# Performance work log

Hardware: AMD Instinct MI355X
Metric: run time of the kernel (lower is better)

The kernel has to match this reference:

```python
import jax, jax.numpy as jnp
import numpy as np

N = 50000      # nodes
E = 800000     # edges
IN = 64        # in_feats
HID = 4        # hidden_size
OUT = 64       # out_feats
COORS = 3
EPS = 1e-07
NEG_SLOPE = 0.01  # F.leaky_relu default


def setup_inputs() -> dict:
    key = jax.random.key(0)
    ks = jax.random.split(key, 10)
    feat = jax.random.normal(ks[0], (N, IN), dtype=jnp.float32)
    pos = jax.random.normal(ks[1], (N, COORS), dtype=jnp.float32)
    src = jax.random.randint(ks[2], (E,), 0, N, dtype=jnp.int32)
    dst = jax.random.randint(ks[3], (E,), 0, N, dtype=jnp.int32)
    W_self = jax.random.normal(ks[4], (OUT, IN), dtype=jnp.float32) * 0.1
    W_sp = jax.random.normal(ks[5], (HID * IN, COORS), dtype=jnp.float32) * 0.3
    b_sp = jax.random.normal(ks[6], (HID * IN,), dtype=jnp.float32) * 0.05
    W_neigh = jax.random.normal(ks[7], (OUT, HID * IN), dtype=jnp.float32) * 0.05
    b_neigh = jax.random.normal(ks[8], (OUT,), dtype=jnp.float32) * 0.05
    bias = jnp.zeros((OUT,), dtype=jnp.float32)
    return {"feat": feat, "pos": pos, "src": src, "dst": dst,
            "W_self": W_self, "W_sp": W_sp, "b_sp": b_sp,
            "W_neigh": W_neigh, "b_neigh": b_neigh, "bias": bias}


def reference(feat, pos, src, dst, W_self, W_sp, b_sp, W_neigh, b_neigh, bias):
    # per-edge spatial weighting
    rel = pos[dst] - pos[src]                                   # [E, 3]
    scal = jnp.linalg.norm(rel, axis=1, keepdims=True) + EPS    # [E, 1]
    ws = (rel + 1.0) / scal                                     # [E, 3]
    s = jax.nn.leaky_relu(ws @ W_sp.T + b_sp, NEG_SLOPE)        # [E, HID*IN]
    # modulate gathered src features: reshape(E, IN, HID) * h_src[:, :, None]
    msg = (s.reshape(E, IN, HID) * feat[src][:, :, None]).reshape(E, IN * HID)
    # mean aggregation per destination node (zero for isolated nodes)
    neigh_sum = jax.ops.segment_sum(msg, dst, num_segments=N)   # [N, IN*HID]
    cnt = jax.ops.segment_sum(jnp.ones((E,), feat.dtype), dst, num_segments=N)
    neigh_h = neigh_sum / jnp.maximum(cnt, 1.0)[:, None]
    # output projections
    h_neigh = neigh_h @ W_neigh.T + b_neigh                     # [N, OUT]
    rst = feat @ W_self.T + h_neigh + bias                      # [N, OUT]
    return rst
```

## Files before the change

kernel.cpp:

```cpp
#include <hip/hip_runtime.h>
#include <math.h>

#define N_NODES 50000
#define N_EDGES 800000
#define EPS 1e-7f
#define NEG_SLOPE 0.01f

#define BUCKET 64
#define EDGE_BLOCKS (N_EDGES / 256)
#define CNT_STRIDE 16

typedef __attribute__((ext_vector_type(8))) short short8;
typedef __attribute__((ext_vector_type(4))) float f32x4;

__device__ __forceinline__ unsigned bf16_rne(float x) {
    unsigned u = __float_as_uint(x);
    u += 0x7fffu + ((u >> 16) & 1u);
    return u >> 16;
}
__device__ __forceinline__ unsigned pack_bf16(float a, float b) {
    return bf16_rne(a) | (bf16_rne(b) << 16);
}


__global__ __launch_bounds__(256) void prep_kernel(
    const int* __restrict__ src, const int* __restrict__ dst,
    const float* __restrict__ pos,
    int* __restrict__ cnt, uint2* __restrict__ gdata,
    const float* __restrict__ W_neigh, const float* __restrict__ W_self,
    const float* __restrict__ b_neigh, const float* __restrict__ bias,
    unsigned* __restrict__ wnp, unsigned* __restrict__ wsp, float* __restrict__ bb)
{
    const int bid = blockIdx.x;

    if (bid == EDGE_BLOCKS) {
        const int t = threadIdx.x;
        const float2* Wn2 = (const float2*)W_neigh;
        const float2* Ws2 = (const float2*)W_self;
        for (int i = t; i < 64 * 128; i += 256) {
            float2 v = Wn2[i];
            wnp[i] = pack_bf16(v.x, v.y);
        }
        for (int i = t; i < 64 * 32; i += 256) {
            float2 v = Ws2[i];
            wsp[i] = pack_bf16(v.x, v.y);
        }
        if (t < 64) bb[t] = b_neigh[t] + bias[t];
        return;
    }

    const int i = bid * 256 + threadIdx.x;
    const int s = src[i], d = dst[i];
    const float sx = pos[s * 3 + 0], sy = pos[s * 3 + 1], sz = pos[s * 3 + 2];
    const float dx = pos[d * 3 + 0], dy = pos[d * 3 + 1], dz = pos[d * 3 + 2];
    const float rx = dx - sx, ry = dy - sy, rz = dz - sz;
    const float inv =
        __builtin_amdgcn_rcpf(__builtin_amdgcn_sqrtf(rx * rx + ry * ry + rz * rz) + EPS);
    const uint2 rec = make_uint2(pack_bf16((rx + 1.f) * inv, (ry + 1.f) * inv),
                                 bf16_rne((rz + 1.f) * inv) | ((unsigned)s << 16));
    const int p = atomicAdd(&cnt[d * CNT_STRIDE], 1);
    if (p < BUCKET) gdata[(size_t)d * BUCKET + p] = rec;
}


#define ACC_STRIDE 264

__device__ __forceinline__ short8 feat_frag_bf16(const float* p) {
    float4 x0 = *reinterpret_cast<const float4*>(p);
    float4 x1 = *reinterpret_cast<const float4*>(p + 4);
    union { unsigned u[4]; short8 s; } c;
    c.u[0] = pack_bf16(x0.x, x0.y);
    c.u[1] = pack_bf16(x0.z, x0.w);
    c.u[2] = pack_bf16(x1.x, x1.y);
    c.u[3] = pack_bf16(x1.z, x1.w);
    return c.s;
}

__global__ __launch_bounds__(256) void aggregate_project_kernel(
    const float* __restrict__ feat, const float* __restrict__ W_sp,
    const float* __restrict__ b_sp, const int* __restrict__ cnt,
    const uint2* __restrict__ gdata, const short* __restrict__ wnb,
    const short* __restrict__ wsb, const float* __restrict__ bb,
    float* __restrict__ out)
{
    __shared__ unsigned short accS[16 * ACC_STRIDE];

    const int lane = threadIdx.x & 63;
    const int w = threadIdx.x >> 6;
    const int nb = blockIdx.x << 4;

    float wsp0[4], wsp1[4], wsp2[4], bsp[4];
#pragma unroll
    for (int h = 0; h < 4; ++h) {
        int j = lane * 4 + h;
        wsp0[h] = W_sp[j * 3 + 0];
        wsp1[h] = W_sp[j * 3 + 1];
        wsp2[h] = W_sp[j * 3 + 2];
        bsp[h]  = b_sp[j];
    }

    for (int q = 0; q < 4; ++q) {
        const int r = (w << 2) + q;
        const int n = nb + r;
        const int degt = __builtin_amdgcn_readfirstlane(cnt[n * CNT_STRIDE]);
        const int deg = min(degt, BUCKET);
        const uint2* gp = gdata + (size_t)n * BUCKET;

        float a0 = 0.f, a1 = 0.f, a2 = 0.f, a3 = 0.f;

        if (deg > 0) {
            const int dm = deg - 1;
            uint2 u0 = gp[0];
            uint2 u1 = gp[min(1, dm)];
            uint2 u2 = gp[min(2, dm)];
            uint2 u3 = gp[min(3, dm)];
            float f0 = feat[(size_t)(u0.y >> 16) * 64 + lane];
            float f1 = feat[(size_t)(u1.y >> 16) * 64 + lane];

            for (int e = 0; e < deg; e += 2) {
                uint2 u4 = gp[min(e + 4, dm)];
                uint2 u5 = gp[min(e + 5, dm)];
                float f2 = feat[(size_t)(u2.y >> 16) * 64 + lane];
                float f3 = feat[(size_t)(u3.y >> 16) * 64 + lane];

                {
                    const float wx = __uint_as_float(u0.x << 16);
                    const float wy = __uint_as_float(u0.x & 0xffff0000u);
                    const float wz = __uint_as_float(u0.y << 16);
                    float t0 = fmaf(wx, wsp0[0], fmaf(wy, wsp1[0], fmaf(wz, wsp2[0], bsp[0])));
                    float t1 = fmaf(wx, wsp0[1], fmaf(wy, wsp1[1], fmaf(wz, wsp2[1], bsp[1])));
                    float t2 = fmaf(wx, wsp0[2], fmaf(wy, wsp1[2], fmaf(wz, wsp2[2], bsp[2])));
                    float t3 = fmaf(wx, wsp0[3], fmaf(wy, wsp1[3], fmaf(wz, wsp2[3], bsp[3])));
                    a0 = fmaf(fmaxf(t0, t0 * NEG_SLOPE), f0, a0);
                    a1 = fmaf(fmaxf(t1, t1 * NEG_SLOPE), f0, a1);
                    a2 = fmaf(fmaxf(t2, t2 * NEG_SLOPE), f0, a2);
                    a3 = fmaf(fmaxf(t3, t3 * NEG_SLOPE), f0, a3);
                }
                {
                    const float m1 = (e + 1 <= dm) ? 1.f : 0.f;
                    const float fm = f1 * m1;
                    const float wx = __uint_as_float(u1.x << 16);
                    const float wy = __uint_as_float(u1.x & 0xffff0000u);
                    const float wz = __uint_as_float(u1.y << 16);
                    float t0 = fmaf(wx, wsp0[0], fmaf(wy, wsp1[0], fmaf(wz, wsp2[0], bsp[0])));
                    float t1 = fmaf(wx, wsp0[1], fmaf(wy, wsp1[1], fmaf(wz, wsp2[1], bsp[1])));
                    float t2 = fmaf(wx, wsp0[2], fmaf(wy, wsp1[2], fmaf(wz, wsp2[2], bsp[2])));
                    float t3 = fmaf(wx, wsp0[3], fmaf(wy, wsp1[3], fmaf(wz, wsp2[3], bsp[3])));
                    a0 = fmaf(fmaxf(t0, t0 * NEG_SLOPE), fm, a0);
                    a1 = fmaf(fmaxf(t1, t1 * NEG_SLOPE), fm, a1);
                    a2 = fmaf(fmaxf(t2, t2 * NEG_SLOPE), fm, a2);
                    a3 = fmaf(fmaxf(t3, t3 * NEG_SLOPE), fm, a3);
                }

                u0 = u2; u1 = u3; u2 = u4; u3 = u5;
                f0 = f2; f1 = f3;
            }
        }

        const float mscale = 1.f / fmaxf((float)degt, 1.f);
        uint2 pv = make_uint2(pack_bf16(a0 * mscale, a1 * mscale),
                              pack_bf16(a2 * mscale, a3 * mscale));
        *reinterpret_cast<uint2*>(&accS[r * ACC_STRIDE + lane * 4]) = pv;
    }
    __syncthreads();

    const int mrow = lane & 15;
    const int quad = lane >> 4;
    const int o = (w << 4) + mrow;

    f32x4 acc = {0.f, 0.f, 0.f, 0.f};

    const unsigned short* Ar = &accS[mrow * ACC_STRIDE + quad * 8];
    const short* Br = wnb + o * 256 + quad * 8;
#pragma unroll
    for (int ks = 0; ks < 8; ++ks) {
        short8 a = *reinterpret_cast<const short8*>(Ar + ks * 32);
        short8 b = *reinterpret_cast<const short8*>(Br + ks * 32);
        acc = __builtin_amdgcn_mfma_f32_16x16x32_bf16(a, b, acc, 0, 0, 0);
    }

    const float* Fr = feat + (size_t)(nb + mrow) * 64 + quad * 8;
    const short* Sr = wsb + o * 64 + quad * 8;
#pragma unroll
    for (int ks = 0; ks < 2; ++ks) {
        short8 a = feat_frag_bf16(Fr + ks * 32);
        short8 b = *reinterpret_cast<const short8*>(Sr + ks * 32);
        acc = __builtin_amdgcn_mfma_f32_16x16x32_bf16(a, b, acc, 0, 0, 0);
    }

    const float badd = bb[o];
#pragma unroll
    for (int r = 0; r < 4; ++r) {
        out[(size_t)(nb + quad * 4 + r) * 64 + o] = acc[r] + badd;
    }
}


extern "C" void kernel_launch(void* const* d_in, const int* in_sizes, int n_in,
                              void* d_out, int out_size, void* d_ws, size_t ws_size,
                              hipStream_t stream) {
    (void)in_sizes; (void)n_in; (void)out_size; (void)ws_size;
    const float* feat    = (const float*)d_in[0];
    const float* pos     = (const float*)d_in[1];
    const int*   src     = (const int*)d_in[2];
    const int*   dst     = (const int*)d_in[3];
    const float* W_self  = (const float*)d_in[4];
    const float* W_sp    = (const float*)d_in[5];
    const float* b_sp    = (const float*)d_in[6];
    const float* W_neigh = (const float*)d_in[7];
    const float* b_neigh = (const float*)d_in[8];
    const float* bias    = (const float*)d_in[9];
    float* out = (float*)d_out;

    uint2*        gdata = (uint2*)d_ws;
    unsigned int* wnp   = (unsigned int*)(gdata + (size_t)N_NODES * BUCKET);
    unsigned int* wsp   = wnp + 8192;
    float*        bb    = (float*)(wsp + 2048);
    int*          cnt   = (int*)(bb + 64);

    hipMemsetAsync(cnt, 0, (size_t)N_NODES * CNT_STRIDE * sizeof(int), stream);
    prep_kernel<<<EDGE_BLOCKS + 1, 256, 0, stream>>>(
        src, dst, pos, cnt, gdata, W_neigh, W_self, b_neigh, bias, wnp, wsp, bb);
    aggregate_project_kernel<<<N_NODES / 16, 256, 0, stream>>>(
        feat, W_sp, b_sp, cnt, gdata, (const short*)wnp, (const short*)wsp, bb, out);
}
```

Baseline: 200.6 us.

## Move edge geometry into aggregation kernel and bucket only source indices

The prep kernel now only atomically buckets source indices (4 bytes per edge) instead of computing and storing packed bf16 geometry records (8 bytes), and the counter array is no longer padded. The aggregation wave loads up to 64 source ids in one coalesced load, computes each edge's relative position and normalization in parallel across lanes, and broadcasts per-edge values with readlane. This cuts scatter write and gather traffic and the pos gathers in prep, at the cost of more atomic contention on unpadded counters and the pos gather moving into the aggregation kernel.

```diff
diff --git a/kernel.cpp b/kernel.cpp
--- a/kernel.cpp
+++ b/kernel.cpp
@@ -8,7 +8,6 @@
 
 #define BUCKET 64
 #define EDGE_BLOCKS (N_EDGES / 256)
-#define CNT_STRIDE 16
 
 typedef __attribute__((ext_vector_type(8))) short short8;
 typedef __attribute__((ext_vector_type(4))) float f32x4;
@@ -25,8 +24,7 @@
 
 __global__ __launch_bounds__(256) void prep_kernel(
     const int* __restrict__ src, const int* __restrict__ dst,
-    const float* __restrict__ pos,
-    int* __restrict__ cnt, uint2* __restrict__ gdata,
+    int* __restrict__ cnt, unsigned* __restrict__ sbuf,
     const float* __restrict__ W_neigh, const float* __restrict__ W_self,
     const float* __restrict__ b_neigh, const float* __restrict__ bias,
     unsigned* __restrict__ wnp, unsigned* __restrict__ wsp, float* __restrict__ bb)
@@ -51,15 +49,8 @@
 
     const int i = bid * 256 + threadIdx.x;
     const int s = src[i], d = dst[i];
-    const float sx = pos[s * 3 + 0], sy = pos[s * 3 + 1], sz = pos[s * 3 + 2];
-    const float dx = pos[d * 3 + 0], dy = pos[d * 3 + 1], dz = pos[d * 3 + 2];
-    const float rx = dx - sx, ry = dy - sy, rz = dz - sz;
-    const float inv =
-        __builtin_amdgcn_rcpf(__builtin_amdgcn_sqrtf(rx * rx + ry * ry + rz * rz) + EPS);
-    const uint2 rec = make_uint2(pack_bf16((rx + 1.f) * inv, (ry + 1.f) * inv),
-                                 bf16_rne((rz + 1.f) * inv) | ((unsigned)s << 16));
-    const int p = atomicAdd(&cnt[d * CNT_STRIDE], 1);
-    if (p < BUCKET) gdata[(size_t)d * BUCKET + p] = rec;
+    const int p = atomicAdd(&cnt[d], 1);
+    if (p < BUCKET) sbuf[(size_t)d * BUCKET + p] = (unsigned)s;
 }
 
 
@@ -77,11 +68,11 @@
 }
 
 __global__ __launch_bounds__(256) void aggregate_project_kernel(
-    const float* __restrict__ feat, const float* __restrict__ W_sp,
-    const float* __restrict__ b_sp, const int* __restrict__ cnt,
-    const uint2* __restrict__ gdata, const short* __restrict__ wnb,
-    const short* __restrict__ wsb, const float* __restrict__ bb,
-    float* __restrict__ out)
+    const float* __restrict__ feat, const float* __restrict__ pos,
+    const float* __restrict__ W_sp, const float* __restrict__ b_sp,
+    const int* __restrict__ cnt, const unsigned* __restrict__ sbuf,
+    const short* __restrict__ wnb, const short* __restrict__ wsb,
+    const float* __restrict__ bb, float* __restrict__ out)
 {
     __shared__ unsigned short accS[16 * ACC_STRIDE];
 
@@ -102,24 +93,41 @@
     for (int q = 0; q < 4; ++q) {
         const int r = (w << 2) + q;
         const int n = nb + r;
-        const int degt = __builtin_amdgcn_readfirstlane(cnt[n * CNT_STRIDE]);
+        const int degt = __builtin_amdgcn_readfirstlane(cnt[n]);
         const int deg = min(degt, BUCKET);
-        const uint2* gp = gdata + (size_t)n * BUCKET;
 
         float a0 = 0.f, a1 = 0.f, a2 = 0.f, a3 = 0.f;
 
         if (deg > 0) {
+            unsigned svr = sbuf[(size_t)n * BUCKET + lane];
+            const unsigned sv = (lane < deg) ? svr : 0u;
+            const float pdx = pos[n * 3 + 0];
+            const float pdy = pos[n * 3 + 1];
+            const float pdz = pos[n * 3 + 2];
+            const float rx = pdx - pos[sv * 3 + 0];
+            const float ry = pdy - pos[sv * 3 + 1];
+            const float rz = pdz - pos[sv * 3 + 2];
+            const float inv =
+                __builtin_amdgcn_rcpf(__builtin_amdgcn_sqrtf(rx * rx + ry * ry + rz * rz) + EPS);
+            const unsigned rx0 = pack_bf16((rx + 1.f) * inv, (ry + 1.f) * inv);
+            const unsigned rx1 = bf16_rne((rz + 1.f) * inv) | (sv << 16);
+
             const int dm = deg - 1;
-            uint2 u0 = gp[0];
-            uint2 u1 = gp[min(1, dm)];
-            uint2 u2 = gp[min(2, dm)];
-            uint2 u3 = gp[min(3, dm)];
+            uint2 u0 = make_uint2((unsigned)__builtin_amdgcn_readlane((int)rx0, 0),
+                                  (unsigned)__builtin_amdgcn_readlane((int)rx1, 0));
+            const int e1i = min(1, dm);
+            uint2 u1 = make_uint2((unsigned)__builtin_amdgcn_readlane((int)rx0, e1i),
+                                  (unsigned)__builtin_amdgcn_readlane((int)rx1, e1i));
             float f0 = feat[(size_t)(u0.y >> 16) * 64 + lane];
             float f1 = feat[(size_t)(u1.y >> 16) * 64 + lane];
 
             for (int e = 0; e < deg; e += 2) {
-                uint2 u4 = gp[min(e + 4, dm)];
-                uint2 u5 = gp[min(e + 5, dm)];
+                const int e2i = min(e + 2, dm);
+                const int e3i = min(e + 3, dm);
+                uint2 u2 = make_uint2((unsigned)__builtin_amdgcn_readlane((int)rx0, e2i),
+                                      (unsigned)__builtin_amdgcn_readlane((int)rx1, e2i));
+                uint2 u3 = make_uint2((unsigned)__builtin_amdgcn_readlane((int)rx0, e3i),
+                                      (unsigned)__builtin_amdgcn_readlane((int)rx1, e3i));
                 float f2 = feat[(size_t)(u2.y >> 16) * 64 + lane];
                 float f3 = feat[(size_t)(u3.y >> 16) * 64 + lane];
 
@@ -152,8 +160,7 @@
                     a3 = fmaf(fmaxf(t3, t3 * NEG_SLOPE), fm, a3);
                 }
 
-                u0 = u2; u1 = u3; u2 = u4; u3 = u5;
-                f0 = f2; f1 = f3;
+                u0 = u2; u1 = u3; f0 = f2; f1 = f3;
             }
         }
 
@@ -212,15 +219,15 @@
     const float* bias    = (const float*)d_in[9];
     float* out = (float*)d_out;
 
-    uint2*        gdata = (uint2*)d_ws;
-    unsigned int* wnp   = (unsigned int*)(gdata + (size_t)N_NODES * BUCKET);
-    unsigned int* wsp   = wnp + 8192;
-    float*        bb    = (float*)(wsp + 2048);
-    int*          cnt   = (int*)(bb + 64);
-
-    hipMemsetAsync(cnt, 0, (size_t)N_NODES * CNT_STRIDE * sizeof(int), stream);
+    unsigned int* sbuf = (unsigned int*)d_ws;
+    unsigned int* wnp  = sbuf + (size_t)N_NODES * BUCKET;
+    unsigned int* wsp  = wnp + 8192;
+    float*        bb   = (float*)(wsp + 2048);
+    int*          cnt  = (int*)(bb + 64);
+
+    hipMemsetAsync(cnt, 0, (size_t)N_NODES * sizeof(int), stream);
     prep_kernel<<<EDGE_BLOCKS + 1, 256, 0, stream>>>(
-        src, dst, pos, cnt, gdata, W_neigh, W_self, b_neigh, bias, wnp, wsp, bb);
+        src, dst, cnt, sbuf, W_neigh, W_self, b_neigh, bias, wnp, wsp, bb);
     aggregate_project_kernel<<<N_NODES / 16, 256, 0, stream>>>(
-        feat, W_sp, b_sp, cnt, gdata, (const short*)wnp, (const short*)wsp, bb, out);
-}
+        feat, pos, W_sp, b_sp, cnt, sbuf, (const short*)wnp, (const short*)wsp, bb, out);
+}
```

Result: no change. 202.3 us (+0.8%).
